# Kernel tuning notes

Measured on AMD Instinct MI355X. Metric: run time of the kernel, lower is better.

Reference implementation:

```python
import jax, jax.numpy as jnp
import numpy as np

D_MODEL = 1024
N_HEAD = 16
D_K = D_MODEL // N_HEAD
B, S = 4, 2048


def setup_inputs() -> dict:
    key = jax.random.key(0)
    ks = jax.random.split(key, 12)
    def w(k):
        return jax.random.normal(k, (D_MODEL, D_MODEL), dtype=jnp.float32) * 0.02
    def b(k):
        return jax.random.normal(k, (D_MODEL,), dtype=jnp.float32) * 0.02
    return {
        "x": jax.random.normal(ks[0], (B, S, D_MODEL), dtype=jnp.float32),
        "pos_emb": jax.random.normal(ks[1], (S, D_MODEL), dtype=jnp.float32),
        "Wq": w(ks[2]), "bq": b(ks[3]),
        "Wk": w(ks[4]), "bk": b(ks[5]),
        "Wv": w(ks[6]), "bv": b(ks[7]),
        "Wp": w(ks[8]), "bp": b(ks[9]),
        "Wo": w(ks[10]), "bo": b(ks[11]),
    }


def reference(x, pos_emb, Wq, bq, Wk, bk, Wv, bv, Wp, bp, Wo, bo):
    # x: [B, S, D]; pos_emb: [S, D]. cache=None path (prefill): kv_len == S.
    Bsz, Sl, _ = x.shape
    def heads(t):  # [B, S, D] -> [B, H, S, dk]
        return t.reshape(Bsz, Sl, N_HEAD, D_K).transpose(0, 2, 1, 3)
    q = heads(x @ Wq.T + bq)
    k = heads(x @ Wk.T + bk)
    v = heads(x @ Wv.T + bv)
    # pos projection: [S, D] -> [H, S, dk]
    p = (pos_emb @ Wp.T + bp).reshape(Sl, N_HEAD, D_K).transpose(1, 0, 2)
    q_pos = q + p[None]  # broadcast over batch
    scores = jnp.einsum("bhqd,bhkd->bhqk", q_pos, k) / jnp.sqrt(jnp.asarray(D_K, x.dtype))
    # causal mask: triu(ones(S, S), diagonal=1) positions are masked
    causal = jnp.tril(jnp.ones((Sl, Sl), dtype=bool))  # True = keep
    scores = jnp.where(causal[None, None], scores, -jnp.inf)
    attn = jax.nn.softmax(scores, axis=-1)  # dropout is identity (eval / p=0)
    out = jnp.einsum("bhqk,bhkd->bhqd", attn, v)
    out = out.transpose(0, 2, 1, 3).reshape(Bsz, Sl, D_MODEL)
    return out @ Wo.T + bo
```

## Files before the change

### kernel.cpp

```cpp
#include <hip/hip_runtime.h>

#define D_MODEL 1024
#define N_HEADS 16
#define DK 64
#define BATCH 4
#define SEQ 2048
#define MROWS (BATCH * SEQ)

typedef float f32x4 __attribute__((ext_vector_type(4)));
typedef short bf16x8 __attribute__((ext_vector_type(8)));
typedef unsigned short u16;
typedef unsigned short u16x8 __attribute__((ext_vector_type(8)));

__device__ __forceinline__ float bf2f(u16 u) {
    union { unsigned int i; float f; } v; v.i = ((unsigned int)u) << 16; return v.f;
}
__device__ __forceinline__ u16 f2bf(float f) {
    union { float f; unsigned int i; } v; v.f = f;
    unsigned int u = v.i;
    u += 0x7fffu + ((u >> 16) & 1u);
    return (u16)(u >> 16);
}
__device__ __forceinline__ unsigned int pk2(float a, float b) {
    union { float f; unsigned int i; } ua, ub; ua.f = a; ub.f = b;
    return __builtin_amdgcn_perm(ub.i + 0x8000u, ua.i + 0x8000u, 0x07060302u);
}

typedef unsigned int u32_as1 __attribute__((address_space(1)));
typedef unsigned int u32_as3 __attribute__((address_space(3)));
__device__ __forceinline__ void gload16(const u16* g, u16* l) {
    __builtin_amdgcn_global_load_lds((const u32_as1*)g, (u32_as3*)l, 16, 0, 0);
}

__global__ __launch_bounds__(256) void convert_all(
    const float* __restrict__ x, const float* __restrict__ pe,
    const float* __restrict__ w0, const float* __restrict__ w1, const float* __restrict__ w2,
    const float* __restrict__ w3, const float* __restrict__ w4,
    u16* __restrict__ xb, u16* __restrict__ pb,
    u16* __restrict__ wb0, u16* __restrict__ wb1, u16* __restrict__ wb2,
    u16* __restrict__ wb3, u16* __restrict__ wb4)
{
    int t = blockIdx.x * 256 + threadIdx.x;
    const float* src; u16* dst; int idx;
    if (t < 1048576)      { src = x;  dst = xb; idx = t; }
    else if (t < 1310720) { src = pe; dst = pb; idx = t - 1048576; }
    else {
        int r = t - 1310720; int w = r >> 17; idx = r & 131071;
        if      (w == 0) { src = w0; dst = wb0; }
        else if (w == 1) { src = w1; dst = wb1; }
        else if (w == 2) { src = w2; dst = wb2; }
        else if (w == 3) { src = w3; dst = wb3; }
        else             { src = w4; dst = wb4; }
    }
    const float4* p = (const float4*)src + (size_t)idx * 2;
    float4 a = p[0], b = p[1];
    u16x8 o;
    o[0] = f2bf(a.x); o[1] = f2bf(a.y); o[2] = f2bf(a.z); o[3] = f2bf(a.w);
    o[4] = f2bf(b.x); o[5] = f2bf(b.y); o[6] = f2bf(b.z); o[7] = f2bf(b.w);
    *((u16x8*)dst + idx) = o;
}

__global__ __launch_bounds__(256) void qkv_gemm(
    const u16* __restrict__ xb, const u16* __restrict__ peb,
    const u16* __restrict__ wqb, const u16* __restrict__ wkb,
    const u16* __restrict__ wvb, const u16* __restrict__ wpb,
    const float* __restrict__ bq, const float* __restrict__ bk,
    const float* __restrict__ bv, const float* __restrict__ bp,
    u16* __restrict__ Qb, u16* __restrict__ Kb, u16* __restrict__ V3,
    u16* __restrict__ Pb)
{
    __shared__ __align__(16) u16 As[128 * 32];
    __shared__ __align__(16) u16 Bs[128 * 32];

    const int tid  = threadIdx.x;
    const int lane = tid & 63;
    const int wv   = tid >> 6;
    const int l15  = lane & 15;
    const int quad = lane >> 4;
    int chunk, m0, n0;
    if (blockIdx.y < 24) {
        chunk = blockIdx.y >> 3; n0 = (blockIdx.y & 7) * 128; m0 = blockIdx.x * 128;
    } else {
        chunk = 3;
        int idx = (blockIdx.y - 24) * 64 + blockIdx.x;
        m0 = (idx & 15) * 128; n0 = ((idx >> 4) & 7) * 128;
    }
    const int wrow = (wv >> 1) * 64;
    const int wcol = (wv & 1) * 64;

    f32x4 acc[4][4];
#pragma unroll
    for (int i = 0; i < 4; ++i)
#pragma unroll
        for (int j = 0; j < 4; ++j) acc[i][j] = f32x4{0.f, 0.f, 0.f, 0.f};

    const int lr = lane >> 2;
    const int lc = (lane & 3) * 8;
    const u16* Abase = (chunk == 3) ? peb : xb;
    const u16* Wbase = (chunk == 0) ? wqb : ((chunk == 1) ? wkb : ((chunk == 2) ? wvb : wpb));
    const u16* Ag = Abase + (size_t)(m0 + wv * 16 + lr) * 1024 + lc;
    const u16* Wg = Wbase + (size_t)(n0 + wv * 16 + lr) * 1024 + lc;
    u16* Al = &As[wv * 16 * 32];
    u16* Bl = &Bs[wv * 16 * 32];

    for (int k0 = 0; k0 < 1024; k0 += 32) {
        __syncthreads();
        gload16(Ag + k0, Al);
        gload16(Ag + (size_t)64 * 1024 + k0, Al + 64 * 32);
        gload16(Wg + k0, Bl);
        gload16(Wg + (size_t)64 * 1024 + k0, Bl + 64 * 32);
        __syncthreads();

        bf16x8 af[4], bfr[4];
#pragma unroll
        for (int i = 0; i < 4; ++i)
            af[i] = *(const bf16x8*)&As[(wrow + 16 * i + l15) * 32 + quad * 8];
#pragma unroll
        for (int j = 0; j < 4; ++j)
            bfr[j] = *(const bf16x8*)&Bs[(wcol + 16 * j + l15) * 32 + quad * 8];
#pragma unroll
        for (int i = 0; i < 4; ++i)
#pragma unroll
            for (int j = 0; j < 4; ++j)
                acc[i][j] = __builtin_amdgcn_mfma_f32_16x16x32_bf16(af[i], bfr[j], acc[i][j], 0, 0, 0);
    }

    const int r0 = quad * 4;
    const float* bias = (chunk == 0) ? bq : ((chunk == 1) ? bk : ((chunk == 2) ? bv : bp));
    u16* dst = (chunk == 0) ? Qb : ((chunk == 1) ? Kb : Pb);
#pragma unroll
    for (int i = 0; i < 4; ++i) {
#pragma unroll
        for (int j = 0; j < 4; ++j) {
            int col = n0 + wcol + 16 * j + l15;
            int row0 = m0 + wrow + 16 * i + r0;
            float bvv = bias[col];
            if (chunk == 2) {
                int hh = col >> 6, d = col & 63;
                int bb = row0 >> 11, sl = row0 & 2047;
                union { u16 h[4]; uint2 v; } pk;
#pragma unroll
                for (int r = 0; r < 4; ++r) pk.h[r] = f2bf(acc[i][j][r] + bvv);
                *((uint2*)V3 + ((size_t)(bb * 16 + hh) * 512 + (sl >> 2)) * 64 + d) = pk.v;
            } else {
#pragma unroll
                for (int r = 0; r < 4; ++r)
                    dst[(size_t)(row0 + r) * 1024 + col] = f2bf(acc[i][j][r] + bvv);
            }
        }
    }
}

__global__ __launch_bounds__(256) void gemm_out(
    const u16* __restrict__ A, const u16* __restrict__ W,
    const float* __restrict__ bias, float* __restrict__ Cout)
{
    __shared__ __align__(16) u16 As[128 * 32];
    __shared__ __align__(16) u16 Bs[128 * 32];

    const int tid  = threadIdx.x;
    const int lane = tid & 63;
    const int wv   = tid >> 6;
    const int l15  = lane & 15;
    const int quad = lane >> 4;
    const int m0   = blockIdx.x * 128;
    const int n0   = blockIdx.y * 128;
    const int wrow = (wv >> 1) * 64;
    const int wcol = (wv & 1) * 64;

    f32x4 acc[4][4];
#pragma unroll
    for (int i = 0; i < 4; ++i)
#pragma unroll
        for (int j = 0; j < 4; ++j) acc[i][j] = f32x4{0.f, 0.f, 0.f, 0.f};

    const int lr = lane >> 2;
    const int lc = (lane & 3) * 8;
    const u16* Ag = A + (size_t)(m0 + wv * 16 + lr) * 1024 + lc;
    const u16* Wg = W + (size_t)(n0 + wv * 16 + lr) * 1024 + lc;
    u16* Al = &As[wv * 16 * 32];
    u16* Bl = &Bs[wv * 16 * 32];

    for (int k0 = 0; k0 < 1024; k0 += 32) {
        __syncthreads();
        gload16(Ag + k0, Al);
        gload16(Ag + 64 * 1024 + k0, Al + 64 * 32);
        gload16(Wg + k0, Bl);
        gload16(Wg + 64 * 1024 + k0, Bl + 64 * 32);
        __syncthreads();

        bf16x8 af[4], bfr[4];
#pragma unroll
        for (int i = 0; i < 4; ++i)
            af[i] = *(const bf16x8*)&As[(wrow + 16 * i + l15) * 32 + quad * 8];
#pragma unroll
        for (int j = 0; j < 4; ++j)
            bfr[j] = *(const bf16x8*)&Bs[(wcol + 16 * j + l15) * 32 + quad * 8];
#pragma unroll
        for (int i = 0; i < 4; ++i)
#pragma unroll
            for (int j = 0; j < 4; ++j)
                acc[i][j] = __builtin_amdgcn_mfma_f32_16x16x32_bf16(af[i], bfr[j], acc[i][j], 0, 0, 0);
    }

    const int r0 = quad * 4;
#pragma unroll
    for (int i = 0; i < 4; ++i)
#pragma unroll
        for (int j = 0; j < 4; ++j) {
            int col = n0 + wcol + 16 * j + l15;
            float bvv = bias[col];
#pragma unroll
            for (int r = 0; r < 4; ++r) {
                int row = m0 + wrow + 16 * i + r0 + r;
                Cout[(size_t)row * 1024 + col] = acc[i][j][r] + bvv;
            }
        }
}

__global__ __launch_bounds__(512, 4) void flash_attn_mfma(
    const u16* __restrict__ Q, const u16* __restrict__ Kq,
    const u16* __restrict__ V3, const u16* __restrict__ Pb, u16* __restrict__ O)
{
    __shared__ __align__(16) u16 Ks[64 * 72];
    __shared__ __align__(16) u16 Vs[64 * 72];
    __shared__ __align__(16) u16 Ps[8][32 * 72];

    const int tid  = threadIdx.x;
    const int lane = tid & 63;
    const int wv   = tid >> 6;
    const int l15  = lane & 15;
    const int quad = lane >> 4;
    const int j    = blockIdx.y;
    const int h    = blockIdx.x & 15;
    const int b    = blockIdx.x >> 4;
    const int qblk = (wv < 4) ? j : (15 - j);
    const int wq0  = qblk * 128 + (wv & 3) * 32;

    bf16x8 qf[2][2];
    const size_t qrowbase = (size_t)(b * SEQ) * D_MODEL + h * DK;
#pragma unroll
    for (int qb = 0; qb < 2; ++qb)
#pragma unroll
        for (int ks = 0; ks < 2; ++ks) {
            int qrow = wq0 + qb * 16 + l15;
            u16x8 qr = *(const u16x8*)(Q + qrowbase + (size_t)qrow * D_MODEL + ks * 32 + quad * 8);
            u16x8 pr = *(const u16x8*)(Pb + (size_t)qrow * D_MODEL + h * DK + ks * 32 + quad * 8);
            u16x8 o;
#pragma unroll
            for (int t = 0; t < 8; ++t)
                o[t] = f2bf((bf2f(qr[t]) + bf2f(pr[t])) * 0.180336880111120f);
            qf[qb][ks] = *(bf16x8*)&o;
        }

    f32x4 Oacc[2][4];
#pragma unroll
    for (int i = 0; i < 2; ++i)
#pragma unroll
        for (int jj = 0; jj < 4; ++jj) Oacc[i][jj] = f32x4{0.f, 0.f, 0.f, 0.f};
    float l_r[2] = {0.f, 0.f};

    const int sr  = tid >> 3;
    const int sc8 = (tid & 7) * 8;
    const u16* Kg = Kq + (size_t)(b * SEQ + sr) * D_MODEL + h * DK + sc8;
    const uint2* Vg = (const uint2*)V3 + ((size_t)(b * 16 + h) * 512 + (tid & 7) * 2) * 64 + sr;
    u16x8 kreg = *(const u16x8*)Kg;
    uint2 v0 = Vg[0], v1 = Vg[64];

    const int ktmaxb = 31 - 2 * j;
    for (int kt = 0; kt <= ktmaxb; ++kt) {
        __syncthreads();
        *(u16x8*)&Ks[sr * 72 + sc8] = kreg;
        *(uint2*)&Vs[sr * 72 + sc8] = v0;
        *(uint2*)&Vs[sr * 72 + sc8 + 4] = v1;
        __syncthreads();
        if (kt < ktmaxb) {
            kreg = *(const u16x8*)(Kg + (size_t)(kt + 1) * 64 * D_MODEL);
            v0 = Vg[(size_t)(kt + 1) * 1024];
            v1 = Vg[(size_t)(kt + 1) * 1024 + 64];
        }
        if (kt * 64 > wq0 + 31) continue;

        f32x4 sacc[4][2];
#pragma unroll
        for (int kb = 0; kb < 4; ++kb)
#pragma unroll
            for (int qb = 0; qb < 2; ++qb) sacc[kb][qb] = f32x4{0.f, 0.f, 0.f, 0.f};
#pragma unroll
        for (int ks = 0; ks < 2; ++ks) {
            bf16x8 kf[4];
#pragma unroll
            for (int kb = 0; kb < 4; ++kb)
                kf[kb] = *(const bf16x8*)&Ks[(kb * 16 + l15) * 72 + ks * 32 + quad * 8];
#pragma unroll
            for (int kb = 0; kb < 4; ++kb)
#pragma unroll
                for (int qb = 0; qb < 2; ++qb)
                    sacc[kb][qb] = __builtin_amdgcn_mfma_f32_16x16x32_bf16(kf[kb], qf[qb][ks], sacc[kb][qb], 0, 0, 0);
        }

        if (kt * 64 + 63 > wq0) {
#pragma unroll
            for (int kb = 0; kb < 4; ++kb) {
                int key_g = kt * 64 + kb * 16 + quad * 4;
#pragma unroll
                for (int qb = 0; qb < 2; ++qb) {
                    int q_g = wq0 + qb * 16 + l15;
#pragma unroll
                    for (int r = 0; r < 4; ++r)
                        if (key_g + r > q_g) sacc[kb][qb][r] = -1e30f;
                }
            }
        }

        u16* Pw = Ps[wv];
#pragma unroll
        for (int qb = 0; qb < 2; ++qb) {
            float s = 0.f;
#pragma unroll
            for (int kb = 0; kb < 4; ++kb) {
                float p0 = __builtin_amdgcn_exp2f(sacc[kb][qb][0]);
                float p1 = __builtin_amdgcn_exp2f(sacc[kb][qb][1]);
                float p2 = __builtin_amdgcn_exp2f(sacc[kb][qb][2]);
                float p3 = __builtin_amdgcn_exp2f(sacc[kb][qb][3]);
                s += (p0 + p1) + (p2 + p3);
                uint2 pk; pk.x = pk2(p0, p1); pk.y = pk2(p2, p3);
                *(uint2*)&Pw[(qb * 16 + l15) * 72 + kb * 16 + quad * 4] = pk;
            }
            l_r[qb] += s;
        }

#pragma unroll
        for (int ks = 0; ks < 2; ++ks) {
            bf16x8 pf[2], vf[4];
#pragma unroll
            for (int qb = 0; qb < 2; ++qb)
                pf[qb] = *(const bf16x8*)&Pw[(qb * 16 + l15) * 72 + ks * 32 + quad * 8];
#pragma unroll
            for (int db = 0; db < 4; ++db)
                vf[db] = *(const bf16x8*)&Vs[(db * 16 + l15) * 72 + ks * 32 + quad * 8];
#pragma unroll
            for (int qb = 0; qb < 2; ++qb)
#pragma unroll
                for (int db = 0; db < 4; ++db)
                    Oacc[qb][db] = __builtin_amdgcn_mfma_f32_16x16x32_bf16(pf[qb], vf[db], Oacc[qb][db], 0, 0, 0);
        }
    }

    float linv[2];
#pragma unroll
    for (int qb = 0; qb < 2; ++qb) {
        float s = l_r[qb];
        s += __shfl_xor(s, 16);
        s += __shfl_xor(s, 32);
        linv[qb] = 1.f / s;
    }
#pragma unroll
    for (int qb = 0; qb < 2; ++qb)
#pragma unroll
        for (int r = 0; r < 4; ++r) {
            float li = __shfl(linv[qb], quad * 4 + r);
            size_t row = (size_t)(b * SEQ + wq0 + qb * 16 + quad * 4 + r) * D_MODEL + h * DK;
#pragma unroll
            for (int db = 0; db < 4; ++db)
                O[row + db * 16 + l15] = f2bf(Oacc[qb][db][r] * li);
        }
}

extern "C" void kernel_launch(void* const* d_in, const int* in_sizes, int n_in,
                              void* d_out, int out_size, void* d_ws, size_t ws_size,
                              hipStream_t stream) {
    const float* x  = (const float*)d_in[0];
    const float* pe = (const float*)d_in[1];
    const float* Wq = (const float*)d_in[2];  const float* bq = (const float*)d_in[3];
    const float* Wk = (const float*)d_in[4];  const float* bk = (const float*)d_in[5];
    const float* Wv = (const float*)d_in[6];  const float* bv = (const float*)d_in[7];
    const float* Wp = (const float*)d_in[8];  const float* bp = (const float*)d_in[9];
    const float* Wo = (const float*)d_in[10]; const float* bo = (const float*)d_in[11];
    float* out = (float*)d_out;
    char* ws = (char*)d_ws;

    size_t off = 0;
    u16* xb  = (u16*)(ws + off); off += (size_t)MROWS * D_MODEL * 2;
    u16* peb = (u16*)(ws + off); off += (size_t)SEQ * D_MODEL * 2;
    u16* wqb = (u16*)(ws + off); off += (size_t)D_MODEL * D_MODEL * 2;
    u16* wkb = (u16*)(ws + off); off += (size_t)D_MODEL * D_MODEL * 2;
    u16* wvb = (u16*)(ws + off); off += (size_t)D_MODEL * D_MODEL * 2;
    u16* wpb = (u16*)(ws + off); off += (size_t)D_MODEL * D_MODEL * 2;
    u16* wob = (u16*)(ws + off); off += (size_t)D_MODEL * D_MODEL * 2;
    u16* Qb  = (u16*)(ws + off); off += (size_t)MROWS * D_MODEL * 2;
    u16* Kb  = (u16*)(ws + off); off += (size_t)MROWS * D_MODEL * 2;
    u16* V3b = (u16*)(ws + off); off += (size_t)MROWS * D_MODEL * 2;
    u16* Pb  = (u16*)(ws + off); off += (size_t)SEQ * D_MODEL * 2;
    u16* AO = xb;

    convert_all<<<7680, 256, 0, stream>>>(x, pe, Wq, Wk, Wv, Wp, Wo,
                                          xb, peb, wqb, wkb, wvb, wpb, wob);

    qkv_gemm<<<dim3(64, 26), 256, 0, stream>>>(
        xb, peb, wqb, wkb, wvb, wpb, bq, bk, bv, bp, Qb, Kb, V3b, Pb);

    flash_attn_mfma<<<dim3(64, 8), 512, 0, stream>>>(Qb, Kb, V3b, Pb, AO);

    gemm_out<<<dim3(64, 8), 256, 0, stream>>>(AO, wob, bo, out);
}
```

Baseline: 305.1 us.

## Rewrite projection GEMMs as 256x256 double-buffered pipelined tiles with swizzled LDS

Both projection GEMMs (fused QKV+pos and output) move from 128x128 single-buffered tiles with two barriers per 32-wide k step to 256x256 tiles over 512 threads. These use 64-wide k slices, double-buffered LDS, interleaved global-to-LDS prefetch between MFMA quarters, XOR-swizzled LDS layout and s_setprio around MFMA bursts. Block IDs are remapped so that neighbouring workgroups share operands in L2. The aim is more data reuse per load, less barrier stall and fewer LDS bank conflicts. In exchange it uses more registers and LDS, and the output GEMM now launches only 128 workgroups, which may leave compute units idle.

```diff
diff --git a/kernel.cpp b/kernel.cpp
--- a/kernel.cpp
+++ b/kernel.cpp
@@ -6,6 +6,7 @@
 #define BATCH 4
 #define SEQ 2048
 #define MROWS (BATCH * SEQ)
+#define TILE_E (256 * 64)
 
 typedef float f32x4 __attribute__((ext_vector_type(4)));
 typedef short bf16x8 __attribute__((ext_vector_type(8)));
@@ -60,7 +61,86 @@
     *((u16x8*)dst + idx) = o;
 }
 
-__global__ __launch_bounds__(256) void qkv_gemm(
+#define SA(bufp, h, kk) do { \
+    gload16(Ag + (size_t)((h) * 64) * 1024 + (kk),       (bufp) + ((h) * 64 + wv * 8) * 64); \
+    gload16(Ag + (size_t)((h) * 64 + 128) * 1024 + (kk), (bufp) + ((h) * 64 + 128 + wv * 8) * 64); \
+} while (0)
+#define SB(bufp, h, kk) do { \
+    gload16(Wg + (size_t)((h) * 32) * 1024 + (kk),       (bufp) + (wq2 * 64 + (h) * 32 + w3 * 8) * 64); \
+    gload16(Wg + (size_t)((h) * 32 + 128) * 1024 + (kk), (bufp) + (128 + wq2 * 64 + (h) * 32 + w3 * 8) * 64); \
+} while (0)
+#define LOAD_A(mh) \
+    _Pragma("unroll") \
+    for (int mi = 0; mi < 4; ++mi) { \
+        aA[mi][0] = *(const bf16x8*)&Abuf[aoff0 + ((mh) * 64 + mi * 16) * 64]; \
+        aA[mi][1] = *(const bf16x8*)&Abuf[aoff1 + ((mh) * 64 + mi * 16) * 64]; \
+    }
+#define LOAD_B(nh) \
+    _Pragma("unroll") \
+    for (int ni = 0; ni < 2; ++ni) { \
+        bB[nh][ni][0] = *(const bf16x8*)&Bbuf[boff0 + ((nh) * 32 + ni * 16) * 64]; \
+        bB[nh][ni][1] = *(const bf16x8*)&Bbuf[boff1 + ((nh) * 32 + ni * 16) * 64]; \
+    }
+#define MFMA16(mh, nh) \
+    _Pragma("unroll") \
+    for (int ks = 0; ks < 2; ++ks) \
+        _Pragma("unroll") \
+        for (int mi = 0; mi < 4; ++mi) \
+            _Pragma("unroll") \
+            for (int ni = 0; ni < 2; ++ni) \
+                acc[(mh) * 4 + mi][(nh) * 2 + ni] = __builtin_amdgcn_mfma_f32_16x16x32_bf16( \
+                    aA[mi][ks], bB[nh][ni][ks], acc[(mh) * 4 + mi][(nh) * 2 + ni], 0, 0, 0);
+
+__device__ __forceinline__ void gemm256_loop(
+    const u16* __restrict__ Ag, const u16* __restrict__ Wg,
+    u16* AsBase, u16* BsBase, int wv,
+    int aoff0, int aoff1, int boff0, int boff1, f32x4 (&acc)[8][4])
+{
+    const int wq2 = wv >> 2, w3 = wv & 3;
+    bf16x8 aA[4][2], bB[2][2][2];
+
+    SA(AsBase, 0, 0); SB(BsBase, 0, 0); SB(BsBase, 1, 0); SA(AsBase, 1, 0);
+    SA(AsBase + TILE_E, 0, 64); SB(BsBase + TILE_E, 0, 64); SA(AsBase + TILE_E, 1, 64);
+    asm volatile("s_waitcnt vmcnt(6)" ::: "memory");
+    __builtin_amdgcn_s_barrier();
+
+    for (int T = 0; T < 16; ++T) {
+        u16* Abuf = AsBase + (T & 1) * TILE_E;
+        u16* Bbuf = BsBase + (T & 1) * TILE_E;
+        u16* Both = BsBase + ((T & 1) ^ 1) * TILE_E;
+        const int k2 = T * 64 + 128;
+
+        LOAD_A(0); LOAD_B(0);
+        if (T < 15) SB(Both, 1, T * 64 + 64);
+        __builtin_amdgcn_s_barrier();
+        asm volatile("s_waitcnt lgkmcnt(0)" ::: "memory");
+        __builtin_amdgcn_s_setprio(1); MFMA16(0, 0); __builtin_amdgcn_s_setprio(0);
+        __builtin_amdgcn_s_barrier();
+
+        LOAD_B(1);
+        if (T < 14) SA(Abuf, 0, k2);
+        __builtin_amdgcn_s_barrier();
+        asm volatile("s_waitcnt lgkmcnt(0)" ::: "memory");
+        __builtin_amdgcn_s_setprio(1); MFMA16(0, 1); __builtin_amdgcn_s_setprio(0);
+        __builtin_amdgcn_s_barrier();
+
+        LOAD_A(1);
+        if (T < 14) SB(Bbuf, 0, k2);
+        __builtin_amdgcn_s_barrier();
+        asm volatile("s_waitcnt lgkmcnt(0)" ::: "memory");
+        __builtin_amdgcn_s_setprio(1); MFMA16(1, 0); __builtin_amdgcn_s_setprio(0);
+        __builtin_amdgcn_s_barrier();
+
+        if (T < 14) SA(Abuf, 1, k2);
+        __builtin_amdgcn_s_barrier();
+        __builtin_amdgcn_s_setprio(1); MFMA16(1, 1); __builtin_amdgcn_s_setprio(0);
+        if (T < 14)      { asm volatile("s_waitcnt vmcnt(6)" ::: "memory"); }
+        else if (T < 15) { asm volatile("s_waitcnt vmcnt(0)" ::: "memory"); }
+        __builtin_amdgcn_s_barrier();
+    }
+}
+
+__global__ __launch_bounds__(512, 2) void qkv_gemm256(
     const u16* __restrict__ xb, const u16* __restrict__ peb,
     const u16* __restrict__ wqb, const u16* __restrict__ wkb,
     const u16* __restrict__ wvb, const u16* __restrict__ wpb,
@@ -69,154 +149,131 @@
     u16* __restrict__ Qb, u16* __restrict__ Kb, u16* __restrict__ V3,
     u16* __restrict__ Pb)
 {
-    __shared__ __align__(16) u16 As[128 * 32];
-    __shared__ __align__(16) u16 Bs[128 * 32];
+    __shared__ __align__(16) u16 As[2 * TILE_E];
+    __shared__ __align__(16) u16 Bs[2 * TILE_E];
 
     const int tid  = threadIdx.x;
     const int lane = tid & 63;
     const int wv   = tid >> 6;
     const int l15  = lane & 15;
     const int quad = lane >> 4;
+    const int wm = wv >> 2, wn = wv & 3;
+
+    int wg = (blockIdx.x & 7) * 52 + (blockIdx.x >> 3);
     int chunk, m0, n0;
-    if (blockIdx.y < 24) {
-        chunk = blockIdx.y >> 3; n0 = (blockIdx.y & 7) * 128; m0 = blockIdx.x * 128;
+    if (wg < 384) {
+        int g = wg >> 5;
+        chunk = g >> 2; n0 = (g & 3) * 256; m0 = (wg & 31) * 256;
     } else {
-        chunk = 3;
-        int idx = (blockIdx.y - 24) * 64 + blockIdx.x;
-        m0 = (idx & 15) * 128; n0 = ((idx >> 4) & 7) * 128;
-    }
-    const int wrow = (wv >> 1) * 64;
-    const int wcol = (wv & 1) * 64;
-
-    f32x4 acc[4][4];
-#pragma unroll
-    for (int i = 0; i < 4; ++i)
-#pragma unroll
-        for (int j = 0; j < 4; ++j) acc[i][j] = f32x4{0.f, 0.f, 0.f, 0.f};
-
-    const int lr = lane >> 2;
-    const int lc = (lane & 3) * 8;
+        int r = wg - 384;
+        chunk = 3; n0 = (r >> 3) * 256; m0 = (r & 7) * 256;
+    }
+
     const u16* Abase = (chunk == 3) ? peb : xb;
     const u16* Wbase = (chunk == 0) ? wqb : ((chunk == 1) ? wkb : ((chunk == 2) ? wvb : wpb));
-    const u16* Ag = Abase + (size_t)(m0 + wv * 16 + lr) * 1024 + lc;
-    const u16* Wg = Wbase + (size_t)(n0 + wv * 16 + lr) * 1024 + lc;
-    u16* Al = &As[wv * 16 * 32];
-    u16* Bl = &Bs[wv * 16 * 32];
-
-    for (int k0 = 0; k0 < 1024; k0 += 32) {
-        __syncthreads();
-        gload16(Ag + k0, Al);
-        gload16(Ag + (size_t)64 * 1024 + k0, Al + 64 * 32);
-        gload16(Wg + k0, Bl);
-        gload16(Wg + (size_t)64 * 1024 + k0, Bl + 64 * 32);
-        __syncthreads();
-
-        bf16x8 af[4], bfr[4];
-#pragma unroll
-        for (int i = 0; i < 4; ++i)
-            af[i] = *(const bf16x8*)&As[(wrow + 16 * i + l15) * 32 + quad * 8];
-#pragma unroll
-        for (int j = 0; j < 4; ++j)
-            bfr[j] = *(const bf16x8*)&Bs[(wcol + 16 * j + l15) * 32 + quad * 8];
-#pragma unroll
-        for (int i = 0; i < 4; ++i)
-#pragma unroll
-            for (int j = 0; j < 4; ++j)
-                acc[i][j] = __builtin_amdgcn_mfma_f32_16x16x32_bf16(af[i], bfr[j], acc[i][j], 0, 0, 0);
-    }
-
-    const int r0 = quad * 4;
+
+    const int trow = tid >> 3;
+    const int swz  = ((tid & 7) ^ (trow & 7)) * 8;
+    const u16* Ag = Abase + (size_t)(m0 + trow) * 1024 + swz;
+    const u16* Wg = Wbase + (size_t)(n0 + (wv >> 2) * 64 + (trow & 31)) * 1024 + swz;
+
+    const int x7 = l15 & 7;
+    const int aoff0 = (wm * 128 + l15) * 64 + ((quad    ) ^ x7) * 8;
+    const int aoff1 = (wm * 128 + l15) * 64 + ((quad + 4) ^ x7) * 8;
+    const int boff0 = (wn * 64 + l15) * 64 + ((quad    ) ^ x7) * 8;
+    const int boff1 = (wn * 64 + l15) * 64 + ((quad + 4) ^ x7) * 8;
+
+    f32x4 acc[8][4];
+#pragma unroll
+    for (int i = 0; i < 8; ++i)
+#pragma unroll
+        for (int j = 0; j < 4; ++j) acc[i][j] = f32x4{0.f, 0.f, 0.f, 0.f};
+
+    gemm256_loop(Ag, Wg, As, Bs, wv, aoff0, aoff1, boff0, boff1, acc);
+
     const float* bias = (chunk == 0) ? bq : ((chunk == 1) ? bk : ((chunk == 2) ? bv : bp));
     u16* dst = (chunk == 0) ? Qb : ((chunk == 1) ? Kb : Pb);
-#pragma unroll
-    for (int i = 0; i < 4; ++i) {
-#pragma unroll
-        for (int j = 0; j < 4; ++j) {
-            int col = n0 + wcol + 16 * j + l15;
-            int row0 = m0 + wrow + 16 * i + r0;
-            float bvv = bias[col];
+    const int r0 = quad * 4;
+#pragma unroll
+    for (int n = 0; n < 4; ++n) {
+        int col = n0 + wn * 64 + n * 16 + l15;
+        float bvv = bias[col];
+#pragma unroll
+        for (int m = 0; m < 8; ++m) {
+            int row0 = m0 + wm * 128 + m * 16 + r0;
             if (chunk == 2) {
                 int hh = col >> 6, d = col & 63;
                 int bb = row0 >> 11, sl = row0 & 2047;
                 union { u16 h[4]; uint2 v; } pk;
 #pragma unroll
-                for (int r = 0; r < 4; ++r) pk.h[r] = f2bf(acc[i][j][r] + bvv);
+                for (int r = 0; r < 4; ++r) pk.h[r] = f2bf(acc[m][n][r] + bvv);
                 *((uint2*)V3 + ((size_t)(bb * 16 + hh) * 512 + (sl >> 2)) * 64 + d) = pk.v;
             } else {
 #pragma unroll
                 for (int r = 0; r < 4; ++r)
-                    dst[(size_t)(row0 + r) * 1024 + col] = f2bf(acc[i][j][r] + bvv);
+                    dst[(size_t)(row0 + r) * 1024 + col] = f2bf(acc[m][n][r] + bvv);
             }
         }
     }
 }
 
-__global__ __launch_bounds__(256) void gemm_out(
+__global__ __launch_bounds__(512, 2) void gemm_out256(
     const u16* __restrict__ A, const u16* __restrict__ W,
     const float* __restrict__ bias, float* __restrict__ Cout)
 {
-    __shared__ __align__(16) u16 As[128 * 32];
-    __shared__ __align__(16) u16 Bs[128 * 32];
+    __shared__ __align__(16) u16 As[2 * TILE_E];
+    __shared__ __align__(16) u16 Bs[2 * TILE_E];
 
     const int tid  = threadIdx.x;
     const int lane = tid & 63;
     const int wv   = tid >> 6;
     const int l15  = lane & 15;
     const int quad = lane >> 4;
-    const int m0   = blockIdx.x * 128;
-    const int n0   = blockIdx.y * 128;
-    const int wrow = (wv >> 1) * 64;
-    const int wcol = (wv & 1) * 64;
-
-    f32x4 acc[4][4];
-#pragma unroll
-    for (int i = 0; i < 4; ++i)
+    const int wm = wv >> 2, wn = wv & 3;
+
+    int wg = (blockIdx.x & 7) * 16 + (blockIdx.x >> 3);
+    const int n0 = (wg >> 5) * 256;
+    const int m0 = (wg & 31) * 256;
+
+    const int trow = tid >> 3;
+    const int swz  = ((tid & 7) ^ (trow & 7)) * 8;
+    const u16* Ag = A + (size_t)(m0 + trow) * 1024 + swz;
+    const u16* Wg = W + (size_t)(n0 + (wv >> 2) * 64 + (trow & 31)) * 1024 + swz;
+
+    const int x7 = l15 & 7;
+    const int aoff0 = (wm * 128 + l15) * 64 + ((quad    ) ^ x7) * 8;
+    const int aoff1 = (wm * 128 + l15) * 64 + ((quad + 4) ^ x7) * 8;
+    const int boff0 = (wn * 64 + l15) * 64 + ((quad    ) ^ x7) * 8;
+    const int boff1 = (wn * 64 + l15) * 64 + ((quad + 4) ^ x7) * 8;
+
+    f32x4 acc[8][4];
+#pragma unroll
+    for (int i = 0; i < 8; ++i)
 #pragma unroll
         for (int j = 0; j < 4; ++j) acc[i][j] = f32x4{0.f, 0.f, 0.f, 0.f};
 
-    const int lr = lane >> 2;
-    const int lc = (lane & 3) * 8;
-    const u16* Ag = A + (size_t)(m0 + wv * 16 + lr) * 1024 + lc;
-    const u16* Wg = W + (size_t)(n0 + wv * 16 + lr) * 1024 + lc;
-    u16* Al = &As[wv * 16 * 32];
-    u16* Bl = &Bs[wv * 16 * 32];
-
-    for (int k0 = 0; k0 < 1024; k0 += 32) {
-        __syncthreads();
-        gload16(Ag + k0, Al);
-        gload16(Ag + 64 * 1024 + k0, Al + 64 * 32);
-        gload16(Wg + k0, Bl);
-        gload16(Wg + 64 * 1024 + k0, Bl + 64 * 32);
-        __syncthreads();
-
-        bf16x8 af[4], bfr[4];
-#pragma unroll
-        for (int i = 0; i < 4; ++i)
-            af[i] = *(const bf16x8*)&As[(wrow + 16 * i + l15) * 32 + quad * 8];
-#pragma unroll
-        for (int j = 0; j < 4; ++j)
-            bfr[j] = *(const bf16x8*)&Bs[(wcol + 16 * j + l15) * 32 + quad * 8];
-#pragma unroll
-        for (int i = 0; i < 4; ++i)
-#pragma unroll
-            for (int j = 0; j < 4; ++j)
-                acc[i][j] = __builtin_amdgcn_mfma_f32_16x16x32_bf16(af[i], bfr[j], acc[i][j], 0, 0, 0);
-    }
+    gemm256_loop(Ag, Wg, As, Bs, wv, aoff0, aoff1, boff0, boff1, acc);
 
     const int r0 = quad * 4;
 #pragma unroll
-    for (int i = 0; i < 4; ++i)
-#pragma unroll
-        for (int j = 0; j < 4; ++j) {
-            int col = n0 + wcol + 16 * j + l15;
-            float bvv = bias[col];
-#pragma unroll
-            for (int r = 0; r < 4; ++r) {
-                int row = m0 + wrow + 16 * i + r0 + r;
-                Cout[(size_t)row * 1024 + col] = acc[i][j][r] + bvv;
-            }
-        }
-}
+    for (int n = 0; n < 4; ++n) {
+        int col = n0 + wn * 64 + n * 16 + l15;
+        float bvv = bias[col];
+#pragma unroll
+        for (int m = 0; m < 8; ++m) {
+            int row0 = m0 + wm * 128 + m * 16 + r0;
+#pragma unroll
+            for (int r = 0; r < 4; ++r)
+                Cout[(size_t)(row0 + r) * 1024 + col] = acc[m][n][r] + bvv;
+        }
+    }
+}
+
+#undef SA
+#undef SB
+#undef LOAD_A
+#undef LOAD_B
+#undef MFMA16
 
 __global__ __launch_bounds__(512, 4) void flash_attn_mfma(
     const u16* __restrict__ Q, const u16* __restrict__ Kq,
@@ -397,10 +454,10 @@
     convert_all<<<7680, 256, 0, stream>>>(x, pe, Wq, Wk, Wv, Wp, Wo,
                                           xb, peb, wqb, wkb, wvb, wpb, wob);
 
-    qkv_gemm<<<dim3(64, 26), 256, 0, stream>>>(
+    qkv_gemm256<<<416, 512, 0, stream>>>(
         xb, peb, wqb, wkb, wvb, wpb, bq, bk, bv, bp, Qb, Kb, V3b, Pb);
 
     flash_attn_mfma<<<dim3(64, 8), 512, 0, stream>>>(Qb, Kb, V3b, Pb, AO);
 
-    gemm_out<<<dim3(64, 8), 256, 0, stream>>>(AO, wob, bo, out);
-}
+    gemm_out256<<<128, 512, 0, stream>>>(AO, wob, bo, out);
+}
```

Result: slower. 311.7 us (+2.1%).
